# Optimization experiments

Measured on AMD Instinct MI355X. Metric: run time of the kernel, lower is better.

Reference implementation:

```python
import jax, jax.numpy as jnp
import numpy as np

NODE_FEATURES = 256
HIDDEN = 32
N_NODES = 100000
N_EDGES = 3200000


def _glorot(key, shape):
    fan_in, fan_out = shape[-2], shape[-1]
    lim = (6.0 / (fan_in + fan_out)) ** 0.5
    return jax.random.uniform(key, shape, jnp.float32, -lim, lim)


def setup_inputs() -> dict:
    key = jax.random.key(0)
    ks = jax.random.split(key, 12)
    in_cat = NODE_FEATURES + HIDDEN  # DConv input is cat([X, H])
    x = jax.random.normal(ks[0], (N_NODES, NODE_FEATURES), jnp.float32)
    edge_index = jax.random.randint(ks[1], (2, N_EDGES), 0, N_NODES, jnp.int64)
    return {
        "x": x,
        "edge_index": edge_index,
        # DConv weights have shape (2, K=1, in, out); squeeze K -> (2, in, out)
        "w_z": _glorot(ks[2], (2, in_cat, HIDDEN)),
        "b_z": jnp.zeros((HIDDEN,), jnp.float32),
        "w_r": _glorot(ks[3], (2, in_cat, HIDDEN)),
        "b_r": jnp.zeros((HIDDEN,), jnp.float32),
        "w_h": _glorot(ks[4], (2, in_cat, HIDDEN)),
        "b_h": jnp.zeros((HIDDEN,), jnp.float32),
        # fc head, stored as [in, out]
        "fc1_w": _glorot(ks[5], (HIDDEN, HIDDEN)),
        "fc1_b": jnp.zeros((HIDDEN,), jnp.float32),
        "fc2_w": _glorot(ks[6], (HIDDEN, 1)),
        "fc2_b": jnp.zeros((1,), jnp.float32),
    }


def _dconv_k1(inp, w, b):
    # K=1 DConv: only the k=0 Chebyshev term for both diffusion directions,
    # i.e. no propagation over edges. H = X @ W_out + X @ W_in + bias.
    return inp @ (w[0] + w[1]) + b


def reference(x, edge_index, w_z, b_z, w_r, b_r, w_h, b_h, fc1_w, fc1_b, fc2_w, fc2_b):
    n = x.shape[0]
    h0 = jnp.zeros((n, HIDDEN), x.dtype)  # DCRNN called with H=None -> zeros
    xh0 = jnp.concatenate([x, h0], axis=1)  # [N, F+H]
    z = jax.nn.sigmoid(_dconv_k1(xh0, w_z, b_z))  # update gate
    r = jax.nn.sigmoid(_dconv_k1(xh0, w_r, b_r))  # reset gate
    xrh = jnp.concatenate([x, r * h0], axis=1)
    h_tilde = jnp.tanh(_dconv_k1(xrh, w_h, b_h))
    h = z * h0 + (1.0 - z) * h_tilde  # [N, 32]
    # fc head: Linear-ReLU-Dropout(eval=identity)-Linear-Sigmoid
    hidden = jax.nn.relu(h @ fc1_w + fc1_b)
    out = jax.nn.sigmoid(hidden @ fc2_w + fc2_b)  # [N, 1]
    return out
```

## Files before the change

kernel.cpp:

```cpp
#include <hip/hip_runtime.h>
#include <hip/hip_bf16.h>


#define NF     256
#define TILE   32
#define WPB    4
#define MB     (TILE * WPB)
#define NTHR   256
#define NCHUNK 16
#define ABUF   2048

typedef __attribute__((ext_vector_type(8)))  short  short8;
typedef __attribute__((ext_vector_type(16))) float  floatx16;

__device__ __forceinline__ unsigned f2bf(float f) {
    __hip_bfloat16 h = __float2bfloat16(f);
    return (unsigned)*(unsigned short*)&h;
}
__device__ __forceinline__ float fast_sigmoid(float v) {
    return 1.0f / (1.0f + __expf(-v));
}
__device__ __forceinline__ float fast_tanh(float v) {
    return 1.0f - 2.0f / (1.0f + __expf(2.0f * v));
}
__device__ __forceinline__ void dma16(const void* g, void* l) {
    __builtin_amdgcn_global_load_lds(
        (const __attribute__((address_space(1))) unsigned int*)g,
        (__attribute__((address_space(3))) unsigned int*)l,
        16, 0, 0);
}

__global__ void prep_W(const float* __restrict__ wz,
                       const float* __restrict__ wh,
                       unsigned short* __restrict__ Wf)
{
    int idx = blockIdx.x * blockDim.x + threadIdx.x;
    if (idx >= NF * 64) return;
    int j    = idx & 7;
    int lane = (idx >> 3) & 63;
    int nt   = (idx >> 9) & 1;
    int kt   = idx >> 10;
    int k = kt * 16 + (lane >> 5) * 8 + j;
    int o = nt * 32 + (lane & 31);
    const int PLANE = 288 * 32;
    float v;
    if (o < 32) v = wz[k * 32 + o]        + wz[PLANE + k * 32 + o];
    else        v = wh[k * 32 + (o - 32)] + wh[PLANE + k * 32 + (o - 32)];
    Wf[idx] = (unsigned short)f2bf(v);
}

__global__ void __launch_bounds__(NTHR, 3)
rgcn_main(const float* __restrict__ x,
          const unsigned short* __restrict__ Wf,
          const float* __restrict__ bz,
          const float* __restrict__ bh,
          const float* __restrict__ fc1w,
          const float* __restrict__ fc1b,
          const float* __restrict__ fc2w,
          const float* __restrict__ fc2b,
          float* __restrict__ out,
          int n_nodes)
{
    __shared__ __align__(16) char SA [WPB * 2 * ABUF];
    __shared__ __align__(16) char SBf[32 * 1024];

    const int tid   = threadIdx.x;
    const int lane  = tid & 63;
    const int wave  = tid >> 6;
    const int node0 = blockIdx.x * MB + wave * TILE;

    {
        const char* wsrc = (const char*)Wf;
#pragma unroll
        for (int i = 0; i < 8; ++i) {
            int g = wave * 8 + i;
            dma16(wsrc + (size_t)g * 1024 + lane * 16, SBf + g * 1024);
        }
    }

    const int nc  = lane & 31;
    const float bzn = bz[nc];
    const float bhn = bh[nc];

    asm volatile("s_waitcnt vmcnt(0)" ::: "memory");
    __syncthreads();

    const int srow = lane >> 2;
    const int slot = (lane & 3) ^ ((lane >> 3) & 3);
    int r0 = node0 + srow;       if (r0 >= n_nodes) r0 = n_nodes - 1;
    int r1 = node0 + 16 + srow;  if (r1 >= n_nodes) r1 = n_nodes - 1;
    const char* a0p = (const char*)x + (size_t)r0 * (NF * 4) + slot * 16;
    const char* a1p = (const char*)x + (size_t)r1 * (NF * 4) + slot * 16;
    char* aw = SA + wave * (2 * ABUF);

    const int m   = lane & 31;
    const int rsw = (m >> 1) & 3;
    const int s0  = (lane >> 5) * 2;
    const int ra0 = m * 64 + (((s0    ) ^ rsw) << 4);
    const int ra1 = m * 64 + (((s0 + 1) ^ rsw) << 4);
    const char* bl = SBf + lane * 16;

    dma16(a0p +  0, aw);          dma16(a1p +  0, aw + 1024);
    dma16(a0p + 64, aw + ABUF);   dma16(a1p + 64, aw + ABUF + 1024);

    floatx16 acc0 = {};
    floatx16 acc1 = {};

#pragma unroll
    for (int c = 0; c < NCHUNK; ++c) {
        if (c < NCHUNK - 1) asm volatile("s_waitcnt vmcnt(2)" ::: "memory");
        else                asm volatile("s_waitcnt vmcnt(0)" ::: "memory");
        __builtin_amdgcn_sched_barrier(0);

        char* ab = aw + (c & 1) * ABUF;
        float4 f0 = *(const float4*)(ab + ra0);
        float4 f1 = *(const float4*)(ab + ra1);
        uint4  vb0 = *(const uint4*)(bl + (size_t)(2 * c    ) * 1024);
        uint4  vb1 = *(const uint4*)(bl + (size_t)(2 * c + 1) * 1024);

        union { short8 s; unsigned u[4]; } A, B0, B1;
        A.u[0] = f2bf(f0.x) | (f2bf(f0.y) << 16);
        A.u[1] = f2bf(f0.z) | (f2bf(f0.w) << 16);
        A.u[2] = f2bf(f1.x) | (f2bf(f1.y) << 16);
        A.u[3] = f2bf(f1.z) | (f2bf(f1.w) << 16);
        B0.u[0] = vb0.x; B0.u[1] = vb0.y; B0.u[2] = vb0.z; B0.u[3] = vb0.w;
        B1.u[0] = vb1.x; B1.u[1] = vb1.y; B1.u[2] = vb1.z; B1.u[3] = vb1.w;

        acc0 = __builtin_amdgcn_mfma_f32_32x32x16_bf16(A.s, B0.s, acc0, 0, 0, 0);
        acc1 = __builtin_amdgcn_mfma_f32_32x32x16_bf16(A.s, B1.s, acc1, 0, 0, 0);

        if (c + 2 < NCHUNK) {
            __builtin_amdgcn_sched_barrier(0);
            dma16(a0p + (size_t)(c + 2) * 64, ab);
            dma16(a1p + (size_t)(c + 2) * 64, ab + 1024);
        }
    }

    float* Hw = (float*)aw;
#pragma unroll
    for (int r = 0; r < 16; ++r) {
        int row = (r & 3) + 8 * (r >> 2) + 4 * (lane >> 5);
        float z = fast_sigmoid(acc0[r] + bzn);
        float t = fast_tanh   (acc1[r] + bhn);
        int boff = row * 128 + ((((nc >> 2) ^ (row & 7)) << 4) | ((nc & 3) << 2));
        *(float*)((char*)Hw + boff) = (1.0f - z) * t;
    }
    asm volatile("s_waitcnt lgkmcnt(0)" ::: "memory");

    const int nl   = lane & 31;
    const int half = lane >> 5;
    float h[32];
#pragma unroll
    for (int q = 0; q < 8; ++q) {
        int boff = nl * 128 + ((q ^ (nl & 7)) << 4);
        float4 v = *(const float4*)((char*)Hw + boff);
        h[q * 4 + 0] = v.x; h[q * 4 + 1] = v.y;
        h[q * 4 + 2] = v.z; h[q * 4 + 3] = v.w;
    }
    float part = 0.0f;
    for (int jj = 0; jj < 16; ++jj) {
        int j = (half << 4) + jj;
        float s = fc1b[j];
#pragma unroll
        for (int o = 0; o < 32; ++o)
            s = fmaf(h[o], fc1w[o * 32 + j], s);
        part = fmaf(fmaxf(s, 0.0f), fc2w[j], part);
    }
    part += __shfl_xor(part, 32);
    if (half == 0) {
        int gn = node0 + nl;
        if (gn < n_nodes)
            out[gn] = fast_sigmoid(part + fc2b[0]);
    }
}

extern "C" void kernel_launch(void* const* d_in, const int* in_sizes, int n_in,
                              void* d_out, int out_size, void* d_ws, size_t ws_size,
                              hipStream_t stream) {
    const float* x    = (const float*)d_in[0];
    const float* wz   = (const float*)d_in[2];
    const float* bz   = (const float*)d_in[3];
    const float* wh   = (const float*)d_in[6];
    const float* bh   = (const float*)d_in[7];
    const float* fc1w = (const float*)d_in[8];
    const float* fc1b = (const float*)d_in[9];
    const float* fc2w = (const float*)d_in[10];
    const float* fc2b = (const float*)d_in[11];
    float* out = (float*)d_out;
    unsigned short* Wf = (unsigned short*)d_ws;

    const int n = in_sizes[0] / NF;

    prep_W<<<(NF * 64 + 255) / 256, 256, 0, stream>>>(wz, wh, Wf);
    rgcn_main<<<(n + MB - 1) / MB, NTHR, 0, stream>>>(
        x, Wf, bz, bh, fc1w, fc1b, fc2w, fc2b, out, n);
}
```

Before: 205.5 us.

## Deepen x-tile prefetch to triple-buffered 128-byte chunks with wider DMA rows

Moves the streaming of x rows into LDS from a double-buffered scheme with 64-byte chunks to a triple-buffered scheme with 128-byte chunks, so each wave keeps more global loads in flight. Each chunk now feeds two MFMA k-steps, and the LDS swizzle and address mapping change to match the 8-slot row layout. This is meant to hide more memory latency on a bandwidth-bound stream of about 100 MB. In exchange, LDS use per block grows and launch bounds drop from 3 to 2 blocks per SM, which lowers occupancy.

```diff
diff --git a/kernel.cpp b/kernel.cpp
--- a/kernel.cpp
+++ b/kernel.cpp
@@ -7,8 +7,9 @@
 #define WPB    4
 #define MB     (TILE * WPB)
 #define NTHR   256
-#define NCHUNK 16
-#define ABUF   2048
+#define NCHUNK 8
+#define NBUF   3
+#define ABUF   4096
 
 typedef __attribute__((ext_vector_type(8)))  short  short8;
 typedef __attribute__((ext_vector_type(16))) float  floatx16;
@@ -49,7 +50,15 @@
     Wf[idx] = (unsigned short)f2bf(v);
 }
 
-__global__ void __launch_bounds__(NTHR, 3)
+#define ISSUE_CHUNK(cc, buf)                                        \
+    do {                                                            \
+        dma16(ap0 + (size_t)(cc) * 128, (buf));                     \
+        dma16(ap1 + (size_t)(cc) * 128, (buf) + 1024);              \
+        dma16(ap2 + (size_t)(cc) * 128, (buf) + 2048);              \
+        dma16(ap3 + (size_t)(cc) * 128, (buf) + 3072);              \
+    } while (0)
+
+__global__ void __launch_bounds__(NTHR, 2)
 rgcn_main(const float* __restrict__ x,
           const unsigned short* __restrict__ Wf,
           const float* __restrict__ bz,
@@ -61,7 +70,7 @@
           float* __restrict__ out,
           int n_nodes)
 {
-    __shared__ __align__(16) char SA [WPB * 2 * ABUF];
+    __shared__ __align__(16) char SA [WPB * NBUF * ABUF];
     __shared__ __align__(16) char SBf[32 * 1024];
 
     const int tid   = threadIdx.x;
@@ -85,54 +94,62 @@
     asm volatile("s_waitcnt vmcnt(0)" ::: "memory");
     __syncthreads();
 
-    const int srow = lane >> 2;
-    const int slot = (lane & 3) ^ ((lane >> 3) & 3);
-    int r0 = node0 + srow;       if (r0 >= n_nodes) r0 = n_nodes - 1;
-    int r1 = node0 + 16 + srow;  if (r1 >= n_nodes) r1 = n_nodes - 1;
-    const char* a0p = (const char*)x + (size_t)r0 * (NF * 4) + slot * 16;
-    const char* a1p = (const char*)x + (size_t)r1 * (NF * 4) + slot * 16;
-    char* aw = SA + wave * (2 * ABUF);
+    const int rg   = lane >> 3;
+    const int gslt = (lane & 7) ^ rg;
+    int r0 = node0 +      rg; if (r0 >= n_nodes) r0 = n_nodes - 1;
+    int r1 = node0 +  8 + rg; if (r1 >= n_nodes) r1 = n_nodes - 1;
+    int r2 = node0 + 16 + rg; if (r2 >= n_nodes) r2 = n_nodes - 1;
+    int r3 = node0 + 24 + rg; if (r3 >= n_nodes) r3 = n_nodes - 1;
+    const char* ap0 = (const char*)x + (size_t)r0 * (NF * 4) + gslt * 16;
+    const char* ap1 = (const char*)x + (size_t)r1 * (NF * 4) + gslt * 16;
+    const char* ap2 = (const char*)x + (size_t)r2 * (NF * 4) + gslt * 16;
+    const char* ap3 = (const char*)x + (size_t)r3 * (NF * 4) + gslt * 16;
+    char* aw = SA + wave * (NBUF * ABUF);
 
     const int m   = lane & 31;
-    const int rsw = (m >> 1) & 3;
-    const int s0  = (lane >> 5) * 2;
-    const int ra0 = m * 64 + (((s0    ) ^ rsw) << 4);
-    const int ra1 = m * 64 + (((s0 + 1) ^ rsw) << 4);
+    const int h   = lane >> 5;
+    const int rsw = m & 7;
     const char* bl = SBf + lane * 16;
 
-    dma16(a0p +  0, aw);          dma16(a1p +  0, aw + 1024);
-    dma16(a0p + 64, aw + ABUF);   dma16(a1p + 64, aw + ABUF + 1024);
+    ISSUE_CHUNK(0, aw);
+    ISSUE_CHUNK(1, aw + ABUF);
+    ISSUE_CHUNK(2, aw + 2 * ABUF);
 
     floatx16 acc0 = {};
     floatx16 acc1 = {};
 
 #pragma unroll
     for (int c = 0; c < NCHUNK; ++c) {
-        if (c < NCHUNK - 1) asm volatile("s_waitcnt vmcnt(2)" ::: "memory");
-        else                asm volatile("s_waitcnt vmcnt(0)" ::: "memory");
+        if (c < 6)       asm volatile("s_waitcnt vmcnt(8)" ::: "memory");
+        else if (c == 6) asm volatile("s_waitcnt vmcnt(4)" ::: "memory");
+        else             asm volatile("s_waitcnt vmcnt(0)" ::: "memory");
         __builtin_amdgcn_sched_barrier(0);
 
-        char* ab = aw + (c & 1) * ABUF;
-        float4 f0 = *(const float4*)(ab + ra0);
-        float4 f1 = *(const float4*)(ab + ra1);
-        uint4  vb0 = *(const uint4*)(bl + (size_t)(2 * c    ) * 1024);
-        uint4  vb1 = *(const uint4*)(bl + (size_t)(2 * c + 1) * 1024);
-
-        union { short8 s; unsigned u[4]; } A, B0, B1;
-        A.u[0] = f2bf(f0.x) | (f2bf(f0.y) << 16);
-        A.u[1] = f2bf(f0.z) | (f2bf(f0.w) << 16);
-        A.u[2] = f2bf(f1.x) | (f2bf(f1.y) << 16);
-        A.u[3] = f2bf(f1.z) | (f2bf(f1.w) << 16);
-        B0.u[0] = vb0.x; B0.u[1] = vb0.y; B0.u[2] = vb0.z; B0.u[3] = vb0.w;
-        B1.u[0] = vb1.x; B1.u[1] = vb1.y; B1.u[2] = vb1.z; B1.u[3] = vb1.w;
-
-        acc0 = __builtin_amdgcn_mfma_f32_32x32x16_bf16(A.s, B0.s, acc0, 0, 0, 0);
-        acc1 = __builtin_amdgcn_mfma_f32_32x32x16_bf16(A.s, B1.s, acc1, 0, 0, 0);
-
-        if (c + 2 < NCHUNK) {
+        char* ab = aw + (c % NBUF) * ABUF;
+#pragma unroll
+        for (int kk = 0; kk < 2; ++kk) {
+            int sA = 4 * kk + 2 * h;
+            float4 f0 = *(const float4*)(ab + m * 128 + (((sA    ) ^ rsw) << 4));
+            float4 f1 = *(const float4*)(ab + m * 128 + (((sA + 1) ^ rsw) << 4));
+            int kt = 2 * c + kk;
+            uint4 b0u = *(const uint4*)(bl + (size_t)(2 * kt    ) * 1024);
+            uint4 b1u = *(const uint4*)(bl + (size_t)(2 * kt + 1) * 1024);
+
+            union { short8 s; unsigned u[4]; } A, B0, B1;
+            A.u[0] = f2bf(f0.x) | (f2bf(f0.y) << 16);
+            A.u[1] = f2bf(f0.z) | (f2bf(f0.w) << 16);
+            A.u[2] = f2bf(f1.x) | (f2bf(f1.y) << 16);
+            A.u[3] = f2bf(f1.z) | (f2bf(f1.w) << 16);
+            B0.u[0] = b0u.x; B0.u[1] = b0u.y; B0.u[2] = b0u.z; B0.u[3] = b0u.w;
+            B1.u[0] = b1u.x; B1.u[1] = b1u.y; B1.u[2] = b1u.z; B1.u[3] = b1u.w;
+
+            acc0 = __builtin_amdgcn_mfma_f32_32x32x16_bf16(A.s, B0.s, acc0, 0, 0, 0);
+            acc1 = __builtin_amdgcn_mfma_f32_32x32x16_bf16(A.s, B1.s, acc1, 0, 0, 0);
+        }
+
+        if (c < NCHUNK - NBUF) {
             __builtin_amdgcn_sched_barrier(0);
-            dma16(a0p + (size_t)(c + 2) * 64, ab);
-            dma16(a1p + (size_t)(c + 2) * 64, ab + 1024);
+            ISSUE_CHUNK(c + NBUF, ab);
         }
     }
 
@@ -149,13 +166,13 @@
 
     const int nl   = lane & 31;
     const int half = lane >> 5;
-    float h[32];
+    float hbuf[32];
 #pragma unroll
     for (int q = 0; q < 8; ++q) {
         int boff = nl * 128 + ((q ^ (nl & 7)) << 4);
         float4 v = *(const float4*)((char*)Hw + boff);
-        h[q * 4 + 0] = v.x; h[q * 4 + 1] = v.y;
-        h[q * 4 + 2] = v.z; h[q * 4 + 3] = v.w;
+        hbuf[q * 4 + 0] = v.x; hbuf[q * 4 + 1] = v.y;
+        hbuf[q * 4 + 2] = v.z; hbuf[q * 4 + 3] = v.w;
     }
     float part = 0.0f;
     for (int jj = 0; jj < 16; ++jj) {
@@ -163,7 +180,7 @@
         float s = fc1b[j];
 #pragma unroll
         for (int o = 0; o < 32; ++o)
-            s = fmaf(h[o], fc1w[o * 32 + j], s);
+            s = fmaf(hbuf[o], fc1w[o * 32 + j], s);
         part = fmaf(fmaxf(s, 0.0f), fc2w[j], part);
     }
     part += __shfl_xor(part, 32);
```

After: 201.6 us. About the same (-1.9%).
